# Optimization experiments

Hardware: AMD Instinct MI355X
Metric: run time of the kernel (lower is better)

## Reference

```python
import jax, jax.numpy as jnp
import numpy as np

NUM_RESIDUES = 2048
CUTOFF = 10.0
POS_SCALE = 30.0

def setup_inputs() -> dict:
    key = jax.random.key(0)
    ks = jax.random.split(key, 7)
    Na, Nb, G = 16384, 16384, 64
    pos_a = jax.random.normal(ks[0], (Na, 3), dtype=jnp.float32) * POS_SCALE
    pos_b = jax.random.normal(ks[1], (Nb, 3), dtype=jnp.float32) * POS_SCALE
    node2graph_a = jnp.sort(jax.random.randint(ks[2], (Na,), 0, G, dtype=jnp.int32))
    node2graph_b = jnp.sort(jax.random.randint(ks[3], (Nb,), 0, G, dtype=jnp.int32))
    atom2residue_a = jax.random.randint(ks[4], (Na,), 0, NUM_RESIDUES, dtype=jnp.int32)
    atom2residue_b = jax.random.randint(ks[5], (Nb,), 0, NUM_RESIDUES, dtype=jnp.int32)
    is_mutation = jax.random.bernoulli(ks[6], 0.01, (Na + Nb,))
    return {"pos_a": pos_a, "pos_b": pos_b,
            "node2graph_a": node2graph_a, "node2graph_b": node2graph_b,
            "atom2residue_a": atom2residue_a, "atom2residue_b": atom2residue_b,
            "is_mutation": is_mutation}

def _interface_mask(dist, atom2residue):
    # scatter_max of (dist < cutoff) per residue, then broadcast back to atoms
    is_iface_atom = (dist < CUTOFF).astype(jnp.int32)
    is_iface_res = jax.ops.segment_max(is_iface_atom, atom2residue,
                                       num_segments=NUM_RESIDUES)
    return is_iface_res[atom2residue] > 0

def reference(pos_a, pos_b, node2graph_a, node2graph_b,
              atom2residue_a, atom2residue_b, is_mutation):
    # segmented pairwise squared distances [Na, Nb] via GEMM expansion
    d2 = (jnp.sum(pos_a * pos_a, -1)[:, None]
          + jnp.sum(pos_b * pos_b, -1)[None, :]
          - 2.0 * (pos_a @ pos_b.T))
    same_graph = node2graph_a[:, None] == node2graph_b[None, :]
    d2 = jnp.where(same_graph, d2, jnp.inf)
    # nearest b for each a, and nearest a for each b (segment-restricted)
    idx_a = jnp.argmin(d2, axis=1)   # [Na]
    idx_b = jnp.argmin(d2, axis=0)   # [Nb]
    dist_a = jnp.linalg.norm(pos_a - pos_b[idx_a], axis=-1)
    dist_b = jnp.linalg.norm(pos_b - pos_a[idx_b], axis=-1)
    mask_a = _interface_mask(dist_a, atom2residue_a)
    mask_b = _interface_mask(dist_b, atom2residue_b)
    mask = jnp.concatenate([mask_a, mask_b]) | is_mutation
    dists = jnp.concatenate([dist_a, dist_b])
    return mask, dists
```

## Files before the change

### kernel.cpp

```cpp
#include <hip/hip_runtime.h>
#include <math.h>

constexpr int   NUM_RES = 2048;
constexpr float CUTOFF  = 10.0f;
constexpr int   NGRAPH  = 64;

__device__ __forceinline__ int lower_bound_i32(const int* __restrict__ arr, int n, int key) {
    int lo = 0, hi = n;
    while (lo < hi) {
        int mid = (lo + hi) >> 1;
        if (arr[mid] < key) lo = mid + 1; else hi = mid;
    }
    return lo;
}

constexpr int WS_FLAGS   = 0;
constexpr int WS_MUTFLAG = 4096;
constexpr int WS_STARTS_A = 4097;
constexpr int WS_STARTS_B = 4162;

__global__ void init_kernel(const unsigned char* __restrict__ mut, int Ntot,
                            const int* __restrict__ n2g_a, int Na,
                            const int* __restrict__ n2g_b, int Nb,
                            int* __restrict__ ws) {
    int tid = blockIdx.x * blockDim.x + threadIdx.x;
    int nthreads = blockDim.x * gridDim.x;

    for (int i = tid; i < 2 * NUM_RES + 1; i += nthreads) ws[WS_FLAGS + i] = 0;

    if (tid >= 8192 && tid < 8192 + (NGRAPH + 1))
        ws[WS_STARTS_A + (tid - 8192)] = lower_bound_i32(n2g_a, Na, tid - 8192);
    if (tid >= 8320 && tid < 8320 + (NGRAPH + 1))
        ws[WS_STARTS_B + (tid - 8320)] = lower_bound_i32(n2g_b, Nb, tid - 8320);

    int acc = 0;
    for (int i = tid; i < Ntot; i += nthreads)
        if ((i & 3) != 0 && mut[i] != 0) acc = 1;
    if (acc) atomicOr(&ws[WS_MUTFLAG], 1);
}

__global__ void __launch_bounds__(256, 8)
nearest_kernel(const float* __restrict__ pos_a,
               const float* __restrict__ pos_b,
               const int* __restrict__ n2g_a,
               const int* __restrict__ n2g_b,
               const int* __restrict__ a2r_a,
               const int* __restrict__ a2r_b,
               int Na, int Nb,
               float* __restrict__ out_dists,
               int* __restrict__ ws) {
    int tid  = blockIdx.x * blockDim.x + threadIdx.x;
    int sub  = tid & 15;
    int atom = tid >> 4;
    int Ntot = Na + Nb;
    if (atom >= Ntot) return;

    const float* ps; const float* po;
    const int* n2g_s; const int* a2r; const int* starts_o;
    int i, side;
    if (atom < Na) {
        side = 0; i = atom;
        ps = pos_a; po = pos_b; n2g_s = n2g_a; a2r = a2r_a;
        starts_o = ws + WS_STARTS_B;
    } else {
        side = 1; i = atom - Na;
        ps = pos_b; po = pos_a; n2g_s = n2g_b; a2r = a2r_b;
        starts_o = ws + WS_STARTS_A;
    }

    float x = ps[3 * i + 0];
    float y = ps[3 * i + 1];
    float z = ps[3 * i + 2];
    int g  = n2g_s[i];
    int r  = a2r[i];
    int lo = starts_o[g];
    int hi = starts_o[g + 1];

    int   best   = 0;
    float bestd2 = INFINITY;
    #pragma unroll 4
    for (int j = lo + sub; j < hi; j += 16) {
        float dx = x - po[3 * j + 0];
        float dy = y - po[3 * j + 1];
        float dz = z - po[3 * j + 2];
        float d2 = dx * dx + dy * dy + dz * dz;
        if (d2 < bestd2) { bestd2 = d2; best = j; }
    }

    for (int off = 8; off >= 1; off >>= 1) {
        float od2 = __shfl_down(bestd2, off, 16);
        int   oj  = __shfl_down(best,   off, 16);
        if (od2 < bestd2 || (od2 == bestd2 && oj < best)) {
            bestd2 = od2; best = oj;
        }
    }

    if (sub == 0) {
        float dx = x - po[3 * best + 0];
        float dy = y - po[3 * best + 1];
        float dz = z - po[3 * best + 2];
        float dist = sqrtf(dx * dx + dy * dy + dz * dz);
        out_dists[atom] = dist;
        if (dist < CUTOFF) {
            ws[WS_FLAGS + side * NUM_RES + r] = 1;
        }
    }
}

__global__ void mask_kernel(const void* __restrict__ mut,
                            const int* __restrict__ a2r_a,
                            const int* __restrict__ a2r_b,
                            int Na, int Nb,
                            const int* __restrict__ ws,
                            float* __restrict__ out_mask) {
    int tid = blockIdx.x * blockDim.x + threadIdx.x;
    int Ntot = Na + Nb;
    if (tid >= Ntot) return;

    int side = (tid < Na) ? 0 : 1;
    int i    = (tid < Na) ? tid : tid - Na;
    int r    = side ? a2r_b[i] : a2r_a[i];
    int iface = ws[WS_FLAGS + side * NUM_RES + r];

    int m;
    if (ws[WS_MUTFLAG]) {
        m = ((const unsigned char*)mut)[tid] != 0;
    } else {
        m = ((const int*)mut)[tid] != 0;
    }
    out_mask[tid] = (iface || m) ? 1.0f : 0.0f;
}

extern "C" void kernel_launch(void* const* d_in, const int* in_sizes, int n_in,
                              void* d_out, int out_size, void* d_ws, size_t ws_size,
                              hipStream_t stream) {
    const float* pos_a = (const float*)d_in[0];
    const float* pos_b = (const float*)d_in[1];
    const int*   n2g_a = (const int*)d_in[2];
    const int*   n2g_b = (const int*)d_in[3];
    const int*   a2r_a = (const int*)d_in[4];
    const int*   a2r_b = (const int*)d_in[5];
    const void*  mut   = d_in[6];

    int Na = in_sizes[0] / 3;
    int Nb = in_sizes[1] / 3;
    int Ntot = Na + Nb;

    float* out = (float*)d_out;
    int* ws = (int*)d_ws;

    init_kernel<<<64, 256, 0, stream>>>((const unsigned char*)mut, Ntot,
                                        n2g_a, Na, n2g_b, Nb, ws);

    int nblocks = (Ntot * 16 + 255) / 256;
    nearest_kernel<<<nblocks, 256, 0, stream>>>(pos_a, pos_b, n2g_a, n2g_b,
                                                a2r_a, a2r_b, Na, Nb,
                                                out + Ntot, ws);

    mask_kernel<<<(Ntot + 255) / 256, 256, 0, stream>>>(mut, a2r_a, a2r_b,
                                                        Na, Nb, ws, out);
}
```

Measured before the change: 78.89 us.

## Fuse init, nearest-neighbor, and mask kernels into one cooperative kernel

Replaces the three separate launches with a single cooperative kernel of 1024 blocks that uses grid-wide syncs between the init, nearest-search and mask phases. Each 16-lane group now loops over atoms grid-stride instead of receiving one atom per launch slot. The aim is to remove launch overhead and gaps between kernels. In exchange it adds the cost of grid.sync, caps the grid size, and lowers the occupancy hint from 8 to 4 waves per SIMD.

```diff
diff --git a/kernel.cpp b/kernel.cpp
--- a/kernel.cpp
+++ b/kernel.cpp
@@ -1,9 +1,17 @@
 #include <hip/hip_runtime.h>
+#include <hip/hip_cooperative_groups.h>
 #include <math.h>
+
+namespace cg = cooperative_groups;
 
 constexpr int   NUM_RES = 2048;
 constexpr float CUTOFF  = 10.0f;
 constexpr int   NGRAPH  = 64;
+
+constexpr int WS_FLAGS    = 0;
+constexpr int WS_MUTFLAG  = 4096;
+constexpr int WS_STARTS_A = 4097;
+constexpr int WS_STARTS_B = 4162;
 
 __device__ __forceinline__ int lower_bound_i32(const int* __restrict__ arr, int n, int key) {
     int lo = 0, hi = n;
@@ -14,121 +22,108 @@
     return lo;
 }
 
-constexpr int WS_FLAGS   = 0;
-constexpr int WS_MUTFLAG = 4096;
-constexpr int WS_STARTS_A = 4097;
-constexpr int WS_STARTS_B = 4162;
-
-__global__ void init_kernel(const unsigned char* __restrict__ mut, int Ntot,
-                            const int* __restrict__ n2g_a, int Na,
-                            const int* __restrict__ n2g_b, int Nb,
-                            int* __restrict__ ws) {
-    int tid = blockIdx.x * blockDim.x + threadIdx.x;
-    int nthreads = blockDim.x * gridDim.x;
+__global__ void __launch_bounds__(256, 4)
+fused_kernel(const float* __restrict__ pos_a, const float* __restrict__ pos_b,
+             const int* __restrict__ n2g_a, const int* __restrict__ n2g_b,
+             const int* __restrict__ a2r_a, const int* __restrict__ a2r_b,
+             const unsigned char* __restrict__ mut,
+             int Na, int Nb,
+             float* __restrict__ out,
+             int* __restrict__ ws)
+{
+    cg::grid_group grid = cg::this_grid();
+    const int tid      = blockIdx.x * blockDim.x + threadIdx.x;
+    const int nthreads = gridDim.x * blockDim.x;
+    const int Ntot     = Na + Nb;
 
     for (int i = tid; i < 2 * NUM_RES + 1; i += nthreads) ws[WS_FLAGS + i] = 0;
-
     if (tid >= 8192 && tid < 8192 + (NGRAPH + 1))
         ws[WS_STARTS_A + (tid - 8192)] = lower_bound_i32(n2g_a, Na, tid - 8192);
     if (tid >= 8320 && tid < 8320 + (NGRAPH + 1))
         ws[WS_STARTS_B + (tid - 8320)] = lower_bound_i32(n2g_b, Nb, tid - 8320);
 
-    int acc = 0;
-    for (int i = tid; i < Ntot; i += nthreads)
-        if ((i & 3) != 0 && mut[i] != 0) acc = 1;
-    if (acc) atomicOr(&ws[WS_MUTFLAG], 1);
-}
+    grid.sync();
 
-__global__ void __launch_bounds__(256, 8)
-nearest_kernel(const float* __restrict__ pos_a,
-               const float* __restrict__ pos_b,
-               const int* __restrict__ n2g_a,
-               const int* __restrict__ n2g_b,
-               const int* __restrict__ a2r_a,
-               const int* __restrict__ a2r_b,
-               int Na, int Nb,
-               float* __restrict__ out_dists,
-               int* __restrict__ ws) {
-    int tid  = blockIdx.x * blockDim.x + threadIdx.x;
-    int sub  = tid & 15;
-    int atom = tid >> 4;
-    int Ntot = Na + Nb;
-    if (atom >= Ntot) return;
-
-    const float* ps; const float* po;
-    const int* n2g_s; const int* a2r; const int* starts_o;
-    int i, side;
-    if (atom < Na) {
-        side = 0; i = atom;
-        ps = pos_a; po = pos_b; n2g_s = n2g_a; a2r = a2r_a;
-        starts_o = ws + WS_STARTS_B;
-    } else {
-        side = 1; i = atom - Na;
-        ps = pos_b; po = pos_a; n2g_s = n2g_b; a2r = a2r_b;
-        starts_o = ws + WS_STARTS_A;
+    {
+        int acc = 0;
+        for (int i = tid; i < Ntot; i += nthreads)
+            if ((i & 3) != 0 && mut[i] != 0) acc = 1;
+        if (acc) atomicOr(&ws[WS_MUTFLAG], 1);
     }
 
-    float x = ps[3 * i + 0];
-    float y = ps[3 * i + 1];
-    float z = ps[3 * i + 2];
-    int g  = n2g_s[i];
-    int r  = a2r[i];
-    int lo = starts_o[g];
-    int hi = starts_o[g + 1];
+    {
+        const int sub     = tid & 15;
+        const int gid     = tid >> 4;
+        const int ngroups = nthreads >> 4;
 
-    int   best   = 0;
-    float bestd2 = INFINITY;
-    #pragma unroll 4
-    for (int j = lo + sub; j < hi; j += 16) {
-        float dx = x - po[3 * j + 0];
-        float dy = y - po[3 * j + 1];
-        float dz = z - po[3 * j + 2];
-        float d2 = dx * dx + dy * dy + dz * dz;
-        if (d2 < bestd2) { bestd2 = d2; best = j; }
-    }
+        for (int a = gid; a < Ntot; a += ngroups) {
+            const float* ps; const float* po;
+            const int* n2g_s; const int* a2r; const int* starts_o;
+            int i, side;
+            if (a < Na) {
+                side = 0; i = a;
+                ps = pos_a; po = pos_b; n2g_s = n2g_a; a2r = a2r_a;
+                starts_o = ws + WS_STARTS_B;
+            } else {
+                side = 1; i = a - Na;
+                ps = pos_b; po = pos_a; n2g_s = n2g_b; a2r = a2r_b;
+                starts_o = ws + WS_STARTS_A;
+            }
 
-    for (int off = 8; off >= 1; off >>= 1) {
-        float od2 = __shfl_down(bestd2, off, 16);
-        int   oj  = __shfl_down(best,   off, 16);
-        if (od2 < bestd2 || (od2 == bestd2 && oj < best)) {
-            bestd2 = od2; best = oj;
+            float x = ps[3 * i + 0];
+            float y = ps[3 * i + 1];
+            float z = ps[3 * i + 2];
+            int g  = n2g_s[i];
+            int r  = a2r[i];
+            int lo = starts_o[g];
+            int hi = starts_o[g + 1];
+
+            int   best   = 0;
+            float bestd2 = INFINITY;
+            #pragma unroll 4
+            for (int j = lo + sub; j < hi; j += 16) {
+                float dx = x - po[3 * j + 0];
+                float dy = y - po[3 * j + 1];
+                float dz = z - po[3 * j + 2];
+                float d2 = dx * dx + dy * dy + dz * dz;
+                if (d2 < bestd2) { bestd2 = d2; best = j; }
+            }
+
+            for (int off = 8; off >= 1; off >>= 1) {
+                float od2 = __shfl_down(bestd2, off, 16);
+                int   oj  = __shfl_down(best,   off, 16);
+                if (od2 < bestd2 || (od2 == bestd2 && oj < best)) {
+                    bestd2 = od2; best = oj;
+                }
+            }
+
+            if (sub == 0) {
+                float dx = x - po[3 * best + 0];
+                float dy = y - po[3 * best + 1];
+                float dz = z - po[3 * best + 2];
+                float dist = sqrtf(dx * dx + dy * dy + dz * dz);
+                out[Ntot + a] = dist;
+                if (dist < CUTOFF) {
+                    ws[WS_FLAGS + side * NUM_RES + r] = 1;
+                }
+            }
         }
     }
 
-    if (sub == 0) {
-        float dx = x - po[3 * best + 0];
-        float dy = y - po[3 * best + 1];
-        float dz = z - po[3 * best + 2];
-        float dist = sqrtf(dx * dx + dy * dy + dz * dz);
-        out_dists[atom] = dist;
-        if (dist < CUTOFF) {
-            ws[WS_FLAGS + side * NUM_RES + r] = 1;
+    grid.sync();
+
+    {
+        const int mutflag = ws[WS_MUTFLAG];
+        for (int t = tid; t < Ntot; t += nthreads) {
+            int side = (t < Na) ? 0 : 1;
+            int i    = (t < Na) ? t : t - Na;
+            int r    = side ? a2r_b[i] : a2r_a[i];
+            int iface = ws[WS_FLAGS + side * NUM_RES + r];
+            int m = mutflag ? (mut[t] != 0)
+                            : (((const int*)mut)[t] != 0);
+            out[t] = (iface || m) ? 1.0f : 0.0f;
         }
     }
-}
-
-__global__ void mask_kernel(const void* __restrict__ mut,
-                            const int* __restrict__ a2r_a,
-                            const int* __restrict__ a2r_b,
-                            int Na, int Nb,
-                            const int* __restrict__ ws,
-                            float* __restrict__ out_mask) {
-    int tid = blockIdx.x * blockDim.x + threadIdx.x;
-    int Ntot = Na + Nb;
-    if (tid >= Ntot) return;
-
-    int side = (tid < Na) ? 0 : 1;
-    int i    = (tid < Na) ? tid : tid - Na;
-    int r    = side ? a2r_b[i] : a2r_a[i];
-    int iface = ws[WS_FLAGS + side * NUM_RES + r];
-
-    int m;
-    if (ws[WS_MUTFLAG]) {
-        m = ((const unsigned char*)mut)[tid] != 0;
-    } else {
-        m = ((const int*)mut)[tid] != 0;
-    }
-    out_mask[tid] = (iface || m) ? 1.0f : 0.0f;
 }
 
 extern "C" void kernel_launch(void* const* d_in, const int* in_sizes, int n_in,
@@ -140,23 +135,22 @@
     const int*   n2g_b = (const int*)d_in[3];
     const int*   a2r_a = (const int*)d_in[4];
     const int*   a2r_b = (const int*)d_in[5];
-    const void*  mut   = d_in[6];
+    const unsigned char* mut = (const unsigned char*)d_in[6];
 
     int Na = in_sizes[0] / 3;
     int Nb = in_sizes[1] / 3;
-    int Ntot = Na + Nb;
 
     float* out = (float*)d_out;
     int* ws = (int*)d_ws;
 
-    init_kernel<<<64, 256, 0, stream>>>((const unsigned char*)mut, Ntot,
-                                        n2g_a, Na, n2g_b, Nb, ws);
-
-    int nblocks = (Ntot * 16 + 255) / 256;
-    nearest_kernel<<<nblocks, 256, 0, stream>>>(pos_a, pos_b, n2g_a, n2g_b,
-                                                a2r_a, a2r_b, Na, Nb,
-                                                out + Ntot, ws);
-
-    mask_kernel<<<(Ntot + 255) / 256, 256, 0, stream>>>(mut, a2r_a, a2r_b,
-                                                        Na, Nb, ws, out);
+    void* args[] = {
+        (void*)&pos_a, (void*)&pos_b,
+        (void*)&n2g_a, (void*)&n2g_b,
+        (void*)&a2r_a, (void*)&a2r_b,
+        (void*)&mut,
+        (void*)&Na, (void*)&Nb,
+        (void*)&out, (void*)&ws
+    };
+    hipLaunchCooperativeKernel((void*)fused_kernel, dim3(1024), dim3(256),
+                               args, 0, stream);
 }
```

Result: slower. 242.2 us (+207.0%).
